# Kernel tuning notes

Measured on AMD Instinct MI355X. Metric: run time of the kernel, lower is better.

The kernel has to match this reference:

```python
import jax, jax.numpy as jnp
import numpy as np

EPS = 1e-5  # torch LayerNorm default
H = 8       # num_heads


def _ln(x, w, b):
    mu = jnp.mean(x, axis=-1, keepdims=True)
    var = jnp.mean(jnp.square(x - mu), axis=-1, keepdims=True)
    return (x - mu) * jax.lax.rsqrt(var + EPS) * w + b


def setup_inputs() -> dict:
    key = jax.random.key(0)
    ks = jax.random.split(key, 8)
    B, N, C = 4, 2048, 512
    d_ff = 4 * C
    g = lambda k, shape: jax.random.normal(k, shape, jnp.float32) * 0.02
    return {
        "x": jax.random.normal(ks[0], (B, N, C), jnp.float32),
        "e": jax.random.normal(ks[1], (B, N, C), jnp.float32),
        "w_qkv": g(ks[2], (C, 3 * C)),
        "w_s": g(ks[3], (C, C)),
        "w_gate": g(ks[4], (C, C)),
        "w_proj": g(ks[5], (C, C)),
        "b_proj": jnp.zeros((C,), jnp.float32),
        "ln1_w": jnp.ones((C,), jnp.float32), "ln1_b": jnp.zeros((C,), jnp.float32),
        "ln2_w": jnp.ones((C,), jnp.float32), "ln2_b": jnp.zeros((C,), jnp.float32),
        "ln3_w": jnp.ones((C,), jnp.float32), "ln3_b": jnp.zeros((C,), jnp.float32),
        "w_fc1": g(ks[6], (C, d_ff)), "b_fc1": jnp.zeros((d_ff,), jnp.float32),
        "w_fc2": g(ks[7], (d_ff, C)), "b_fc2": jnp.zeros((C,), jnp.float32),
    }


def reference(x, e, w_qkv, w_s, w_gate, w_proj, b_proj,
              ln1_w, ln1_b, ln2_w, ln2_b, ln3_w, ln3_b,
              w_fc1, b_fc1, w_fc2, b_fc2):
    B, N, C = x.shape
    D = C // H
    scale = D ** -0.5  # qk_scale=None -> (dim//num_heads)**-0.5

    # --- attention branch: x + attn(norm1(x), norm2(e)) ---
    xn = _ln(x, ln1_w, ln1_b)
    en = _ln(e, ln2_w, ln2_b)
    qkv = (xn @ w_qkv).reshape(B, N, 3, H, D).transpose(2, 0, 3, 1, 4)  # [3,B,H,N,D]
    q, k, v = qkv[0], qkv[1], qkv[2]
    s = (en @ w_s).reshape(B, N, H, D).transpose(0, 2, 1, 3)            # [B,H,N,D]
    attn = jax.nn.softmax(jnp.einsum('bhnd,bhmd->bhnm', q, k + s) * scale, axis=-1)
    o = jnp.einsum('bhnm,bhmd->bhnd', attn, v).transpose(0, 2, 1, 3).reshape(B, N, C)
    o = (o * (xn @ w_gate)) @ w_proj + b_proj
    x = x + o  # drop_path is identity (drop_prob=0)

    # --- MLP branch: x + mlp(norm3(x)) ---
    xn3 = _ln(x, ln3_w, ln3_b)
    h = jax.nn.gelu(xn3 @ w_fc1 + b_fc1, approximate=False)  # torch nn.GELU = exact erf
    return x + (h @ w_fc2 + b_fc2)
```

## Files before the change

### kernel.cpp

```cpp
#include <hip/hip_runtime.h>

typedef unsigned short u16;
typedef short s16;
typedef u16 u16x4 __attribute__((ext_vector_type(4)));
typedef u16 u16x8 __attribute__((ext_vector_type(8)));
typedef s16 s16x8 __attribute__((ext_vector_type(8)));
typedef float f32x4 __attribute__((ext_vector_type(4)));

__device__ __forceinline__ float b2f(u16 u) {
  union { unsigned int i; float f; } v;
  v.i = ((unsigned int)u) << 16;
  return v.f;
}
__device__ __forceinline__ u16 f2b(float f) {
  union { float f; unsigned int i; } v;
  v.f = f;
  unsigned int r = v.i + 0x7fffu + ((v.i >> 16) & 1u);
  return (u16)(r >> 16);
}

#define MFMA16(a, b, c) __builtin_amdgcn_mfma_f32_16x16x32_bf16(a, b, c, 0, 0, 0)

__device__ __forceinline__ void gld16(const u16* g, u16* l) {
  __builtin_amdgcn_global_load_lds(
      (const __attribute__((address_space(1))) void*)g,
      (__attribute__((address_space(3))) void*)l, 16, 0, 0);
}

__global__ __launch_bounds__(256) void ln12_kernel(
    const float* __restrict__ x, const float* __restrict__ e,
    const float* __restrict__ w1, const float* __restrict__ b1,
    const float* __restrict__ w2, const float* __restrict__ b2,
    u16* __restrict__ xn, u16* __restrict__ en) {
  int bid = blockIdx.x;
  const float *inv, *w, *bb;
  u16* out;
  if (bid < 2048) { inv = x; w = w1; bb = b1; out = xn; }
  else { bid -= 2048; inv = e; w = w2; bb = b2; out = en; }
  const int row = bid * 4 + (threadIdx.x >> 6);
  const int lane = threadIdx.x & 63;
  const float* p = inv + (size_t)row * 512 + lane * 8;
  f32x4 v0 = *(const f32x4*)p;
  f32x4 v1 = *(const f32x4*)(p + 4);
  float xv[8];
#pragma unroll
  for (int i = 0; i < 4; i++) { xv[i] = v0[i]; xv[4 + i] = v1[i]; }
  float s = 0.f;
#pragma unroll
  for (int i = 0; i < 8; i++) s += xv[i];
#pragma unroll
  for (int m = 1; m < 64; m <<= 1) s += __shfl_xor(s, m, 64);
  const float mu = s * (1.0f / 512.0f);
  float vs = 0.f;
#pragma unroll
  for (int i = 0; i < 8; i++) { const float d = xv[i] - mu; vs += d * d; }
#pragma unroll
  for (int m = 1; m < 64; m <<= 1) vs += __shfl_xor(vs, m, 64);
  const float r = rsqrtf(vs * (1.0f / 512.0f) + 1e-5f);
  const f32x4 w0 = *(const f32x4*)(w + lane * 8);
  const f32x4 w1v = *(const f32x4*)(w + lane * 8 + 4);
  const f32x4 bb0 = *(const f32x4*)(bb + lane * 8);
  const f32x4 bb1 = *(const f32x4*)(bb + lane * 8 + 4);
  u16x8 ov;
#pragma unroll
  for (int i = 0; i < 4; i++) {
    ov[i] = f2b((xv[i] - mu) * r * w0[i] + bb0[i]);
    ov[4 + i] = f2b((xv[4 + i] - mu) * r * w1v[i] + bb1[i]);
  }
  *(u16x8*)(out + (size_t)row * 512 + lane * 8) = ov;
}

__global__ __launch_bounds__(256) void ln_kernel(const float* __restrict__ inv,
                                                 const float* __restrict__ w,
                                                 const float* __restrict__ bvec,
                                                 u16* __restrict__ out) {
  const int row = blockIdx.x * 4 + (threadIdx.x >> 6);
  const int lane = threadIdx.x & 63;
  const float* p = inv + (size_t)row * 512 + lane * 8;
  f32x4 v0 = *(const f32x4*)p;
  f32x4 v1 = *(const f32x4*)(p + 4);
  float x[8];
#pragma unroll
  for (int i = 0; i < 4; i++) { x[i] = v0[i]; x[4 + i] = v1[i]; }
  float s = 0.f;
#pragma unroll
  for (int i = 0; i < 8; i++) s += x[i];
#pragma unroll
  for (int m = 1; m < 64; m <<= 1) s += __shfl_xor(s, m, 64);
  const float mu = s * (1.0f / 512.0f);
  float vs = 0.f;
#pragma unroll
  for (int i = 0; i < 8; i++) { const float d = x[i] - mu; vs += d * d; }
#pragma unroll
  for (int m = 1; m < 64; m <<= 1) vs += __shfl_xor(vs, m, 64);
  const float r = rsqrtf(vs * (1.0f / 512.0f) + 1e-5f);
  const f32x4 w0 = *(const f32x4*)(w + lane * 8);
  const f32x4 w1 = *(const f32x4*)(w + lane * 8 + 4);
  const f32x4 b0 = *(const f32x4*)(bvec + lane * 8);
  const f32x4 b1 = *(const f32x4*)(bvec + lane * 8 + 4);
  u16x8 ov;
#pragma unroll
  for (int i = 0; i < 4; i++) {
    ov[i] = f2b((x[i] - mu) * r * w0[i] + b0[i]);
    ov[4 + i] = f2b((x[4 + i] - mu) * r * w1[i] + b1[i]);
  }
  *(u16x8*)(out + (size_t)row * 512 + lane * 8) = ov;
}

__global__ __launch_bounds__(256) void wprep_kernel(
    const float* __restrict__ wq, const float* __restrict__ wsc,
    const float* __restrict__ wg, const float* __restrict__ wp,
    const float* __restrict__ w1, const float* __restrict__ w2,
    u16* __restrict__ wqgT, u16* __restrict__ wsT, u16* __restrict__ wpT,
    u16* __restrict__ wf1T, u16* __restrict__ wf2T) {
  __shared__ float T[64][65];
  int bid = blockIdx.x;
  const float* src; u16* dst; int K, N, ntiles;
  if (bid < 192)      { src = wq;  dst = wqgT;              K = 512;  N = 1536; ntiles = 24; }
  else if (bid < 256) { src = wg;  dst = wqgT + 1536 * 512; K = 512;  N = 512;  ntiles = 8; bid -= 192; }
  else if (bid < 320) { src = wsc; dst = wsT;               K = 512;  N = 512;  ntiles = 8; bid -= 256; }
  else if (bid < 384) { src = wp;  dst = wpT;               K = 512;  N = 512;  ntiles = 8; bid -= 320; }
  else if (bid < 640) { src = w1;  dst = wf1T;              K = 512;  N = 2048; ntiles = 32; bid -= 384; }
  else                { src = w2;  dst = wf2T;              K = 2048; N = 512;  ntiles = 8; bid -= 640; }
  const int n0 = (bid % ntiles) * 64, k0 = (bid / ntiles) * 64;
  const int c = threadIdx.x & 63, r0 = threadIdx.x >> 6;
#pragma unroll
  for (int i = 0; i < 16; i++) {
    const int r = i * 4 + r0;
    T[r][c] = src[(size_t)(k0 + r) * N + n0 + c];
  }
  __syncthreads();
#pragma unroll
  for (int i = 0; i < 16; i++) {
    const int r = i * 4 + r0;
    dst[(size_t)(n0 + r) * K + k0 + c] = f2b(T[c][r]);
  }
}

enum { EPI_NONE = 0, EPI_F32RES = 1, EPI_GELU = 2 };

template<int EPI, int BM>
__global__ __launch_bounds__(256) void mgemm(const u16* __restrict__ A,
                                             const u16* __restrict__ Bt,
                                             int M, int N, int K,
                                             u16* __restrict__ Cb, float* Cf,
                                             const float* __restrict__ bias,
                                             const float* resf) {
  constexpr int NT = (BM == 128) ? 4 : 2;
  constexpr int ACH = BM / 32;
  __shared__ u16 As[BM * 64];
  __shared__ u16 Bs[128 * 64];
  const int tid = threadIdx.x;
  const int wv = tid >> 6, lane = tid & 63;
  const int quad = lane >> 4, l16 = lane & 15;
  const int sw = l16 & 7;
  const int wrow = (BM == 128) ? (wv >> 1) * 64 : 0;
  const int wcol = (BM == 128) ? (wv & 1) * 64 : wv * 32;
  const int m0 = blockIdx.y * BM, n0 = blockIdx.x * 128;
  const int lrow = lane >> 3;
  const int lcs = ((lane & 7) ^ lrow) * 8;
  f32x4 acc[4][NT];
#pragma unroll
  for (int i = 0; i < 4; i++)
#pragma unroll
    for (int j = 0; j < NT; j++) acc[i][j] = (f32x4){0.f, 0.f, 0.f, 0.f};
  for (int k0 = 0; k0 < K; k0 += 64) {
    __syncthreads();
#pragma unroll
    for (int i = 0; i < ACH; i++) {
      const int ch = wv * ACH + i;
      gld16(A + (size_t)(m0 + ch * 8 + lrow) * K + k0 + lcs, &As[ch * 512]);
    }
#pragma unroll
    for (int i = 0; i < 4; i++) {
      const int ch = wv * 4 + i;
      gld16(Bt + (size_t)(n0 + ch * 8 + lrow) * K + k0 + lcs, &Bs[ch * 512]);
    }
    __syncthreads();
#pragma unroll
    for (int ks = 0; ks < 2; ks++) {
      s16x8 af[4], bf[NT];
#pragma unroll
      for (int mt = 0; mt < 4; mt++)
        af[mt] = *(const s16x8*)&As[(wrow + mt * 16 + l16) * 64 +
                                    (((ks * 4 + quad) ^ sw) * 8)];
#pragma unroll
      for (int nt = 0; nt < NT; nt++)
        bf[nt] = *(const s16x8*)&Bs[(wcol + nt * 16 + l16) * 64 +
                                    (((ks * 4 + quad) ^ sw) * 8)];
#pragma unroll
      for (int mt = 0; mt < 4; mt++)
#pragma unroll
        for (int nt = 0; nt < NT; nt++)
          acc[mt][nt] = MFMA16(af[mt], bf[nt], acc[mt][nt]);
    }
  }
#pragma unroll
  for (int nt = 0; nt < NT; nt++) {
    const int n = n0 + wcol + nt * 16 + l16;
    const float bn = (EPI != EPI_NONE) ? bias[n] : 0.f;
#pragma unroll
    for (int mt = 0; mt < 4; mt++) {
#pragma unroll
      for (int r = 0; r < 4; r++) {
        const int m = m0 + wrow + mt * 16 + quad * 4 + r;
        float v = acc[mt][nt][r] + bn;
        if (EPI == EPI_GELU)
          v = 0.5f * v * (1.0f + erff(v * 0.70710678118654752f));
        if (EPI == EPI_F32RES) {
          const size_t idx = (size_t)m * N + n;
          Cf[idx] = v + resf[idx];
        } else {
          Cb[(size_t)m * N + n] = f2b(v);
        }
      }
    }
  }
}

__global__ __launch_bounds__(256) void ksvt_kernel(const u16* __restrict__ qg,
                                                   const u16* __restrict__ sb,
                                                   u16* __restrict__ ksg,
                                                   u16* __restrict__ vtg) {
  __shared__ u16 T[64 * 72];
  const int bh = blockIdx.y;
  const int b = bh >> 3, h = bh & 7;
  const int kk0 = blockIdx.x * 64;
  const size_t rb = (size_t)b * 2048;
  const size_t base = (size_t)bh * 131072;
  const int row = threadIdx.x >> 2, cb = (threadIdx.x & 3) * 16;
  const u16* kp = qg + (rb + kk0 + row) * 2048 + 512 + h * 64 + cb;
  const u16* sp = sb + (rb + kk0 + row) * 512 + h * 64 + cb;
  const u16x8 k0v = *(const u16x8*)kp;
  const u16x8 k1v = *(const u16x8*)(kp + 8);
  const u16x8 s0v = *(const u16x8*)sp;
  const u16x8 s1v = *(const u16x8*)(sp + 8);
  u16x8 o0, o1;
#pragma unroll
  for (int i = 0; i < 8; i++) {
    o0[i] = f2b(b2f(k0v[i]) + b2f(s0v[i]));
    o1[i] = f2b(b2f(k1v[i]) + b2f(s1v[i]));
  }
  *(u16x8*)(ksg + base + (size_t)(kk0 + row) * 64 + cb) = o0;
  *(u16x8*)(ksg + base + (size_t)(kk0 + row) * 64 + cb + 8) = o1;
  const u16x8 v0v = *(const u16x8*)(kp + 512);
  const u16x8 v1v = *(const u16x8*)(kp + 520);
  *(u16x8*)&T[row * 72 + cb] = v0v;
  *(u16x8*)&T[row * 72 + cb + 8] = v1v;
  __syncthreads();
  u16x8 a0, a1;
#pragma unroll
  for (int i = 0; i < 8; i++) {
    a0[i] = T[(cb + i) * 72 + row];
    a1[i] = T[(cb + 8 + i) * 72 + row];
  }
  *(u16x8*)(vtg + base + (size_t)row * 2048 + kk0 + cb) = a0;
  *(u16x8*)(vtg + base + (size_t)row * 2048 + kk0 + cb + 8) = a1;
}

__global__ __launch_bounds__(256) void attn_kernel(const u16* __restrict__ qg,
                                                   const u16* __restrict__ ksg,
                                                   const u16* __restrict__ vtg,
                                                   u16* __restrict__ og) {
  __shared__ u16 KSs[64 * 64];
  __shared__ u16 VTs[64 * 64];
  __shared__ u16 PS[4][16 * 72];
  const int tid = threadIdx.x;
  const int w = tid >> 6, lane = tid & 63;
  const int quad = lane >> 4, l16 = lane & 15;
  const int sw = l16 & 7;
  const int q0 = blockIdx.x * 64;
  const int bh = blockIdx.y;
  const int h = bh & 7;
  const size_t rb = (size_t)(bh >> 3) * 2048;
  const size_t base = (size_t)bh * 131072;
  const int lrow = lane >> 3;
  const int lcs = ((lane & 7) ^ lrow) * 8;

  s16x8 aq[2];
  {
    const u16* qp = qg + (rb + q0 + w * 16 + l16) * 2048 + h * 64 + quad * 8;
#pragma unroll
    for (int ks = 0; ks < 2; ks++) {
      const u16x8 qv = *(const u16x8*)(qp + ks * 32);
      s16x8 t;
#pragma unroll
      for (int i = 0; i < 8; i++) t[i] = (s16)f2b(b2f(qv[i]) * 0.125f);
      aq[ks] = t;
    }
  }
  float m_run = -1e30f, l_run = 0.f;
  f32x4 oacc[4];
#pragma unroll
  for (int nt = 0; nt < 4; nt++) oacc[nt] = (f32x4){0.f, 0.f, 0.f, 0.f};

  for (int kt = 0; kt < 32; kt++) {
    const int kk0 = kt * 64;
    __syncthreads();
#pragma unroll
    for (int i = 0; i < 2; i++) {
      const int ch = w * 2 + i;
      gld16(ksg + base + (size_t)(kk0 + ch * 8 + lrow) * 64 + lcs, &KSs[ch * 512]);
      gld16(vtg + base + (size_t)(ch * 8 + lrow) * 2048 + kk0 + lcs, &VTs[ch * 512]);
    }
    __syncthreads();
    f32x4 sacc[4];
#pragma unroll
    for (int mt = 0; mt < 4; mt++) sacc[mt] = (f32x4){0.f, 0.f, 0.f, 0.f};
#pragma unroll
    for (int ks = 0; ks < 2; ks++) {
#pragma unroll
      for (int mt = 0; mt < 4; mt++) {
        const s16x8 kf = *(const s16x8*)&KSs[(mt * 16 + l16) * 64 +
                                             (((ks * 4 + quad) ^ sw) * 8)];
        sacc[mt] = MFMA16(kf, aq[ks], sacc[mt]);
      }
    }
    float lm = -1e30f;
#pragma unroll
    for (int mt = 0; mt < 4; mt++)
#pragma unroll
      for (int r = 0; r < 4; r++) lm = fmaxf(lm, sacc[mt][r]);
    lm = fmaxf(lm, __shfl_xor(lm, 16, 64));
    lm = fmaxf(lm, __shfl_xor(lm, 32, 64));
    const float mn = fmaxf(m_run, lm);
    const float alpha = __expf(m_run - mn);
    m_run = mn;
    float ls = 0.f;
#pragma unroll
    for (int mt = 0; mt < 4; mt++) {
#pragma unroll
      for (int r = 0; r < 4; r++) {
        const float pv = __expf(sacc[mt][r] - mn);
        sacc[mt][r] = pv;
        ls += pv;
      }
    }
    ls += __shfl_xor(ls, 16, 64);
    ls += __shfl_xor(ls, 32, 64);
    l_run = l_run * alpha + ls;
#pragma unroll
    for (int mt = 0; mt < 4; mt++) {
      u16x4 pk;
#pragma unroll
      for (int r = 0; r < 4; r++) pk[r] = f2b(sacc[mt][r]);
      *(u16x4*)&PS[w][l16 * 72 + mt * 16 + quad * 4] = pk;
    }
#pragma unroll
    for (int r = 0; r < 4; r++) {
      const float af = __shfl(alpha, quad * 4 + r, 64);
#pragma unroll
      for (int nt = 0; nt < 4; nt++) oacc[nt][r] *= af;
    }
#pragma unroll
    for (int ks = 0; ks < 2; ks++) {
      const s16x8 pf = *(const s16x8*)&PS[w][l16 * 72 + ks * 32 + quad * 8];
#pragma unroll
      for (int nt = 0; nt < 4; nt++) {
        const s16x8 vf = *(const s16x8*)&VTs[(nt * 16 + l16) * 64 +
                                             (((ks * 4 + quad) ^ sw) * 8)];
        oacc[nt] = MFMA16(pf, vf, oacc[nt]);
      }
    }
  }
#pragma unroll
  for (int r = 0; r < 4; r++) {
    const float linv = 1.0f / __shfl(l_run, quad * 4 + r, 64);
    const size_t grow = (rb + q0 + w * 16 + quad * 4 + r) * 2048 + 1536 + h * 64;
    const size_t rowb = (rb + q0 + w * 16 + quad * 4 + r) * 512 + h * 64;
#pragma unroll
    for (int nt = 0; nt < 4; nt++) {
      const float g = b2f(qg[grow + nt * 16 + l16]);
      og[rowb + nt * 16 + l16] = f2b(oacc[nt][r] * linv * g);
    }
  }
}

extern "C" void kernel_launch(void* const* d_in, const int* in_sizes, int n_in,
                              void* d_out, int out_size, void* d_ws, size_t ws_size,
                              hipStream_t stream) {
  const float* x      = (const float*)d_in[0];
  const float* e      = (const float*)d_in[1];
  const float* w_qkv  = (const float*)d_in[2];
  const float* w_s    = (const float*)d_in[3];
  const float* w_gate = (const float*)d_in[4];
  const float* w_proj = (const float*)d_in[5];
  const float* b_proj = (const float*)d_in[6];
  const float* ln1w   = (const float*)d_in[7];
  const float* ln1b   = (const float*)d_in[8];
  const float* ln2w   = (const float*)d_in[9];
  const float* ln2b   = (const float*)d_in[10];
  const float* ln3w   = (const float*)d_in[11];
  const float* ln3b   = (const float*)d_in[12];
  const float* w_fc1  = (const float*)d_in[13];
  const float* b_fc1  = (const float*)d_in[14];
  const float* w_fc2  = (const float*)d_in[15];
  const float* b_fc2  = (const float*)d_in[16];
  float* out = (float*)d_out;
  char* ws = (char*)d_ws;

  u16* xn    = (u16*)(ws + 0);
  u16* en    = (u16*)(ws + 8388608);
  u16* qg    = (u16*)(ws + 16777216);
  u16* sbuf  = (u16*)(ws + 50331648);
  u16* obuf  = (u16*)(ws + 58720256);
  u16* wqgT  = (u16*)(ws + 67108864);
  u16* wsT   = (u16*)(ws + 69206016);
  u16* wpT   = (u16*)(ws + 69730304);
  u16* wf1T  = (u16*)(ws + 70254592);
  u16* wf2T  = (u16*)(ws + 72351744);
  u16* vtg   = (u16*)(ws + 74448896);
  u16* ksg   = en;
  u16* hbuf  = qg;
  u16* xn3   = xn;

  dim3 blk(256);
  wprep_kernel<<<896, blk, 0, stream>>>(w_qkv, w_s, w_gate, w_proj, w_fc1, w_fc2,
                                        wqgT, wsT, wpT, wf1T, wf2T);
  ln12_kernel<<<4096, blk, 0, stream>>>(x, e, ln1w, ln1b, ln2w, ln2b, xn, en);
  mgemm<EPI_NONE, 128><<<dim3(16, 64), blk, 0, stream>>>(
      xn, wqgT, 8192, 2048, 512, qg, nullptr, nullptr, nullptr);
  mgemm<EPI_NONE, 64><<<dim3(4, 128), blk, 0, stream>>>(
      en, wsT, 8192, 512, 512, sbuf, nullptr, nullptr, nullptr);
  ksvt_kernel<<<dim3(32, 32), blk, 0, stream>>>(qg, sbuf, ksg, vtg);
  attn_kernel<<<dim3(32, 32), blk, 0, stream>>>(qg, ksg, vtg, obuf);
  mgemm<EPI_F32RES, 64><<<dim3(4, 128), blk, 0, stream>>>(
      obuf, wpT, 8192, 512, 512, nullptr, out, b_proj, x);
  ln_kernel<<<2048, blk, 0, stream>>>(out, ln3w, ln3b, xn3);
  mgemm<EPI_GELU, 128><<<dim3(16, 64), blk, 0, stream>>>(
      xn3, wf1T, 8192, 2048, 512, hbuf, nullptr, b_fc1, nullptr);
  mgemm<EPI_F32RES, 64><<<dim3(4, 128), blk, 0, stream>>>(
      hbuf, wf2T, 8192, 512, 2048, nullptr, out, b_fc2, out);
  (void)in_sizes; (void)n_in; (void)out_size; (void)ws_size;
}
```

Before: 351.1 us.

## Fuse k+s add into s-GEMM epilogue, double-buffer attention K/V, BK=128 for narrow GEMMs

```diff
diff --git a/kernel.cpp b/kernel.cpp
--- a/kernel.cpp
+++ b/kernel.cpp
@@ -137,19 +137,23 @@
   }
 }
 
-enum { EPI_NONE = 0, EPI_F32RES = 1, EPI_GELU = 2 };
-
-template<int EPI, int BM>
+enum { EPI_NONE = 0, EPI_F32RES = 1, EPI_GELU = 2, EPI_KS = 3 };
+
+template<int EPI, int BM, int BK>
 __global__ __launch_bounds__(256) void mgemm(const u16* __restrict__ A,
                                              const u16* __restrict__ Bt,
                                              int M, int N, int K,
                                              u16* __restrict__ Cb, float* Cf,
                                              const float* __restrict__ bias,
-                                             const float* resf) {
+                                             const float* resf,
+                                             const u16* __restrict__ kq) {
   constexpr int NT = (BM == 128) ? 4 : 2;
-  constexpr int ACH = BM / 32;
-  __shared__ u16 As[BM * 64];
-  __shared__ u16 Bs[128 * 64];
+  constexpr int ACHW = BM * BK / 512 / 4;
+  constexpr int BCHW = 128 * BK / 512 / 4;
+  constexpr int LPR = BK / 8;
+  constexpr int RPC = 512 / BK;
+  __shared__ u16 As[BM * BK];
+  __shared__ u16 Bs[128 * BK];
   const int tid = threadIdx.x;
   const int wv = tid >> 6, lane = tid & 63;
   const int quad = lane >> 4, l16 = lane & 15;
@@ -157,36 +161,38 @@
   const int wrow = (BM == 128) ? (wv >> 1) * 64 : 0;
   const int wcol = (BM == 128) ? (wv & 1) * 64 : wv * 32;
   const int m0 = blockIdx.y * BM, n0 = blockIdx.x * 128;
-  const int lrow = lane >> 3;
-  const int lcs = ((lane & 7) ^ lrow) * 8;
+  const int lrow = lane / LPR;
+  const int inrow = lane % LPR;
   f32x4 acc[4][NT];
 #pragma unroll
   for (int i = 0; i < 4; i++)
 #pragma unroll
     for (int j = 0; j < NT; j++) acc[i][j] = (f32x4){0.f, 0.f, 0.f, 0.f};
-  for (int k0 = 0; k0 < K; k0 += 64) {
+  for (int k0 = 0; k0 < K; k0 += BK) {
     __syncthreads();
 #pragma unroll
-    for (int i = 0; i < ACH; i++) {
-      const int ch = wv * ACH + i;
-      gld16(A + (size_t)(m0 + ch * 8 + lrow) * K + k0 + lcs, &As[ch * 512]);
-    }
-#pragma unroll
-    for (int i = 0; i < 4; i++) {
-      const int ch = wv * 4 + i;
-      gld16(Bt + (size_t)(n0 + ch * 8 + lrow) * K + k0 + lcs, &Bs[ch * 512]);
+    for (int i = 0; i < ACHW; i++) {
+      const int ch = wv * ACHW + i;
+      const int r = ch * RPC + lrow;
+      gld16(A + (size_t)(m0 + r) * K + k0 + ((inrow ^ (r & 7)) * 8), &As[ch * 512]);
+    }
+#pragma unroll
+    for (int i = 0; i < BCHW; i++) {
+      const int ch = wv * BCHW + i;
+      const int r = ch * RPC + lrow;
+      gld16(Bt + (size_t)(n0 + r) * K + k0 + ((inrow ^ (r & 7)) * 8), &Bs[ch * 512]);
     }
     __syncthreads();
 #pragma unroll
-    for (int ks = 0; ks < 2; ks++) {
+    for (int ks = 0; ks < BK / 32; ks++) {
       s16x8 af[4], bf[NT];
 #pragma unroll
       for (int mt = 0; mt < 4; mt++)
-        af[mt] = *(const s16x8*)&As[(wrow + mt * 16 + l16) * 64 +
+        af[mt] = *(const s16x8*)&As[(wrow + mt * 16 + l16) * BK +
                                     (((ks * 4 + quad) ^ sw) * 8)];
 #pragma unroll
       for (int nt = 0; nt < NT; nt++)
-        bf[nt] = *(const s16x8*)&Bs[(wcol + nt * 16 + l16) * 64 +
+        bf[nt] = *(const s16x8*)&Bs[(wcol + nt * 16 + l16) * BK +
                                     (((ks * 4 + quad) ^ sw) * 8)];
 #pragma unroll
       for (int mt = 0; mt < 4; mt++)
@@ -198,7 +204,7 @@
 #pragma unroll
   for (int nt = 0; nt < NT; nt++) {
     const int n = n0 + wcol + nt * 16 + l16;
-    const float bn = (EPI != EPI_NONE) ? bias[n] : 0.f;
+    const float bn = (EPI == EPI_F32RES || EPI == EPI_GELU) ? bias[n] : 0.f;
 #pragma unroll
     for (int mt = 0; mt < 4; mt++) {
 #pragma unroll
@@ -210,6 +216,10 @@
         if (EPI == EPI_F32RES) {
           const size_t idx = (size_t)m * N + n;
           Cf[idx] = v + resf[idx];
+        } else if (EPI == EPI_KS) {
+          v += b2f(kq[(size_t)m * 2048 + 512 + n]);
+          const int b = m >> 11, kk = m & 2047, h = n >> 6, d = n & 63;
+          Cb[(size_t)(b * 8 + h) * 131072 + (size_t)kk * 64 + d] = f2b(v);
         } else {
           Cb[(size_t)m * N + n] = f2b(v);
         }
@@ -218,10 +228,8 @@
   }
 }
 
-__global__ __launch_bounds__(256) void ksvt_kernel(const u16* __restrict__ qg,
-                                                   const u16* __restrict__ sb,
-                                                   u16* __restrict__ ksg,
-                                                   u16* __restrict__ vtg) {
+__global__ __launch_bounds__(256) void vt_kernel(const u16* __restrict__ qg,
+                                                 u16* __restrict__ vtg) {
   __shared__ u16 T[64 * 72];
   const int bh = blockIdx.y;
   const int b = bh >> 3, h = bh & 7;
@@ -229,22 +237,9 @@
   const size_t rb = (size_t)b * 2048;
   const size_t base = (size_t)bh * 131072;
   const int row = threadIdx.x >> 2, cb = (threadIdx.x & 3) * 16;
-  const u16* kp = qg + (rb + kk0 + row) * 2048 + 512 + h * 64 + cb;
-  const u16* sp = sb + (rb + kk0 + row) * 512 + h * 64 + cb;
-  const u16x8 k0v = *(const u16x8*)kp;
-  const u16x8 k1v = *(const u16x8*)(kp + 8);
-  const u16x8 s0v = *(const u16x8*)sp;
-  const u16x8 s1v = *(const u16x8*)(sp + 8);
-  u16x8 o0, o1;
-#pragma unroll
-  for (int i = 0; i < 8; i++) {
-    o0[i] = f2b(b2f(k0v[i]) + b2f(s0v[i]));
-    o1[i] = f2b(b2f(k1v[i]) + b2f(s1v[i]));
-  }
-  *(u16x8*)(ksg + base + (size_t)(kk0 + row) * 64 + cb) = o0;
-  *(u16x8*)(ksg + base + (size_t)(kk0 + row) * 64 + cb + 8) = o1;
-  const u16x8 v0v = *(const u16x8*)(kp + 512);
-  const u16x8 v1v = *(const u16x8*)(kp + 520);
+  const u16* vp = qg + (rb + kk0 + row) * 2048 + 1024 + h * 64 + cb;
+  const u16x8 v0v = *(const u16x8*)vp;
+  const u16x8 v1v = *(const u16x8*)(vp + 8);
   *(u16x8*)&T[row * 72 + cb] = v0v;
   *(u16x8*)&T[row * 72 + cb + 8] = v1v;
   __syncthreads();
@@ -262,8 +257,8 @@
                                                    const u16* __restrict__ ksg,
                                                    const u16* __restrict__ vtg,
                                                    u16* __restrict__ og) {
-  __shared__ u16 KSs[64 * 64];
-  __shared__ u16 VTs[64 * 64];
+  __shared__ u16 KSs[2][64 * 64];
+  __shared__ u16 VTs[2][64 * 64];
   __shared__ u16 PS[4][16 * 72];
   const int tid = threadIdx.x;
   const int w = tid >> 6, lane = tid & 63;
@@ -294,16 +289,26 @@
 #pragma unroll
   for (int nt = 0; nt < 4; nt++) oacc[nt] = (f32x4){0.f, 0.f, 0.f, 0.f};
 
+  const int ch0 = w * 2, ch1 = w * 2 + 1;
+  {
+    gld16(ksg + base + (size_t)(ch0 * 8 + lrow) * 64 + lcs, &KSs[0][ch0 * 512]);
+    gld16(ksg + base + (size_t)(ch1 * 8 + lrow) * 64 + lcs, &KSs[0][ch1 * 512]);
+    gld16(vtg + base + (size_t)(ch0 * 8 + lrow) * 2048 + lcs, &VTs[0][ch0 * 512]);
+    gld16(vtg + base + (size_t)(ch1 * 8 + lrow) * 2048 + lcs, &VTs[0][ch1 * 512]);
+  }
+
   for (int kt = 0; kt < 32; kt++) {
-    const int kk0 = kt * 64;
+    const int cur = kt & 1;
     __syncthreads();
-#pragma unroll
-    for (int i = 0; i < 2; i++) {
-      const int ch = w * 2 + i;
-      gld16(ksg + base + (size_t)(kk0 + ch * 8 + lrow) * 64 + lcs, &KSs[ch * 512]);
-      gld16(vtg + base + (size_t)(ch * 8 + lrow) * 2048 + kk0 + lcs, &VTs[ch * 512]);
-    }
-    __syncthreads();
+    if (kt < 31) {
+      const int nk0 = (kt + 1) * 64;
+      u16* kd = (u16*)KSs[cur ^ 1];
+      u16* vd = (u16*)VTs[cur ^ 1];
+      gld16(ksg + base + (size_t)(nk0 + ch0 * 8 + lrow) * 64 + lcs, &kd[ch0 * 512]);
+      gld16(ksg + base + (size_t)(nk0 + ch1 * 8 + lrow) * 64 + lcs, &kd[ch1 * 512]);
+      gld16(vtg + base + (size_t)(ch0 * 8 + lrow) * 2048 + nk0 + lcs, &vd[ch0 * 512]);
+      gld16(vtg + base + (size_t)(ch1 * 8 + lrow) * 2048 + nk0 + lcs, &vd[ch1 * 512]);
+    }
     f32x4 sacc[4];
 #pragma unroll
     for (int mt = 0; mt < 4; mt++) sacc[mt] = (f32x4){0.f, 0.f, 0.f, 0.f};
@@ -311,8 +316,8 @@
     for (int ks = 0; ks < 2; ks++) {
 #pragma unroll
       for (int mt = 0; mt < 4; mt++) {
-        const s16x8 kf = *(const s16x8*)&KSs[(mt * 16 + l16) * 64 +
-                                             (((ks * 4 + quad) ^ sw) * 8)];
+        const s16x8 kf = *(const s16x8*)&KSs[cur][(mt * 16 + l16) * 64 +
+                                                 (((ks * 4 + quad) ^ sw) * 8)];
         sacc[mt] = MFMA16(kf, aq[ks], sacc[mt]);
       }
     }
@@ -357,8 +362,8 @@
       const s16x8 pf = *(const s16x8*)&PS[w][l16 * 72 + ks * 32 + quad * 8];
 #pragma unroll
       for (int nt = 0; nt < 4; nt++) {
-        const s16x8 vf = *(const s16x8*)&VTs[(nt * 16 + l16) * 64 +
-                                             (((ks * 4 + quad) ^ sw) * 8)];
+        const s16x8 vf = *(const s16x8*)&VTs[cur][(nt * 16 + l16) * 64 +
+                                                  (((ks * 4 + quad) ^ sw) * 8)];
         oacc[nt] = MFMA16(pf, vf, oacc[nt]);
       }
     }
@@ -366,12 +371,13 @@
 #pragma unroll
   for (int r = 0; r < 4; r++) {
     const float linv = 1.0f / __shfl(l_run, quad * 4 + r, 64);
-    const size_t grow = (rb + q0 + w * 16 + quad * 4 + r) * 2048 + 1536 + h * 64;
-    const size_t rowb = (rb + q0 + w * 16 + quad * 4 + r) * 512 + h * 64;
+    const size_t qrow = rb + q0 + w * 16 + quad * 4 + r;
+    const size_t grow = qrow * 2048 + 1536 + h * 64;
+    const size_t rowb = qrow * 512 + h * 64;
 #pragma unroll
     for (int nt = 0; nt < 4; nt++) {
-      const float g = b2f(qg[grow + nt * 16 + l16]);
-      og[rowb + nt * 16 + l16] = f2b(oacc[nt][r] * linv * g);
+      const float gv = b2f(qg[grow + nt * 16 + l16]);
+      og[rowb + nt * 16 + l16] = f2b(oacc[nt][r] * linv * gv);
     }
   }
 }
@@ -402,7 +408,7 @@
   u16* xn    = (u16*)(ws + 0);
   u16* en    = (u16*)(ws + 8388608);
   u16* qg    = (u16*)(ws + 16777216);
-  u16* sbuf  = (u16*)(ws + 50331648);
+  u16* ksg   = (u16*)(ws + 50331648);
   u16* obuf  = (u16*)(ws + 58720256);
   u16* wqgT  = (u16*)(ws + 67108864);
   u16* wsT   = (u16*)(ws + 69206016);
@@ -410,7 +416,6 @@
   u16* wf1T  = (u16*)(ws + 70254592);
   u16* wf2T  = (u16*)(ws + 72351744);
   u16* vtg   = (u16*)(ws + 74448896);
-  u16* ksg   = en;
   u16* hbuf  = qg;
   u16* xn3   = xn;
 
@@ -418,18 +423,18 @@
   wprep_kernel<<<896, blk, 0, stream>>>(w_qkv, w_s, w_gate, w_proj, w_fc1, w_fc2,
                                         wqgT, wsT, wpT, wf1T, wf2T);
   ln12_kernel<<<4096, blk, 0, stream>>>(x, e, ln1w, ln1b, ln2w, ln2b, xn, en);
-  mgemm<EPI_NONE, 128><<<dim3(16, 64), blk, 0, stream>>>(
-      xn, wqgT, 8192, 2048, 512, qg, nullptr, nullptr, nullptr);
-  mgemm<EPI_NONE, 64><<<dim3(4, 128), blk, 0, stream>>>(
-      en, wsT, 8192, 512, 512, sbuf, nullptr, nullptr, nullptr);
-  ksvt_kernel<<<dim3(32, 32), blk, 0, stream>>>(qg, sbuf, ksg, vtg);
+  mgemm<EPI_NONE, 128, 64><<<dim3(16, 64), blk, 0, stream>>>(
+      xn, wqgT, 8192, 2048, 512, qg, nullptr, nullptr, nullptr, nullptr);
+  mgemm<EPI_KS, 64, 128><<<dim3(4, 128), blk, 0, stream>>>(
+      en, wsT, 8192, 512, 512, ksg, nullptr, nullptr, nullptr, qg);
+  vt_kernel<<<dim3(32, 32), blk, 0, stream>>>(qg, vtg);
   attn_kernel<<<dim3(32, 32), blk, 0, stream>>>(qg, ksg, vtg, obuf);
-  mgemm<EPI_F32RES, 64><<<dim3(4, 128), blk, 0, stream>>>(
-      obuf, wpT, 8192, 512, 512, nullptr, out, b_proj, x);
+  mgemm<EPI_F32RES, 64, 128><<<dim3(4, 128), blk, 0, stream>>>(
+      obuf, wpT, 8192, 512, 512, nullptr, out, b_proj, x, nullptr);
   ln_kernel<<<2048, blk, 0, stream>>>(out, ln3w, ln3b, xn3);
-  mgemm<EPI_GELU, 128><<<dim3(16, 64), blk, 0, stream>>>(
-      xn3, wf1T, 8192, 2048, 512, hbuf, nullptr, b_fc1, nullptr);
-  mgemm<EPI_F32RES, 64><<<dim3(4, 128), blk, 0, stream>>>(
-      hbuf, wf2T, 8192, 512, 2048, nullptr, out, b_fc2, out);
+  mgemm<EPI_GELU, 128, 64><<<dim3(16, 64), blk, 0, stream>>>(
+      xn3, wf1T, 8192, 2048, 512, hbuf, nullptr, b_fc1, nullptr, nullptr);
+  mgemm<EPI_F32RES, 64, 128><<<dim3(4, 128), blk, 0, stream>>>(
+      hbuf, wf2T, 8192, 512, 2048, nullptr, out, b_fc2, out, nullptr);
   (void)in_sizes; (void)n_in; (void)out_size; (void)ws_size;
 }
```

After: 358.9 us. 1.02x slower.
